# Performance work log

Hardware: AMD Instinct MI355X
Metric: run time of the kernel (lower is better)

## Reference

```python
import jax, jax.numpy as jnp
import numpy as np

E = 640000   # n_edges
D = 128      # feature_dim
N = 40000    # n_dst_nodes


def setup_inputs() -> dict:
    key = jax.random.key(0)
    k1, k2, k3 = jax.random.split(key, 3)
    src_emb = jax.random.normal(k1, (E, D), dtype=jnp.float32)
    dst_idx = jax.random.randint(k2, (E,), 0, N, dtype=jnp.int64)
    # nn.Linear default init scale ~ 1/sqrt(fan_in)
    W = jax.random.normal(k3, (D, D), dtype=jnp.float32) / jnp.sqrt(jnp.float32(D))
    b = jnp.zeros((D,), dtype=jnp.float32)
    return {"src_emb": src_emb, "W": W, "b": b, "dst_idx": dst_idx, "n_nodes": N}


def reference(src_emb, W, b, dst_idx, n_nodes):
    # msg_e = relu(Linear(src_emb))  -- per-edge messages [E, D]
    msg = jax.nn.relu(jnp.einsum("ed,fd->ef", src_emb, W) + b)
    # update_all(copy_edge, max) == segment max over destination nodes [N, D]
    h_node = jax.ops.segment_max(msg, dst_idx, num_segments=n_nodes)
    return h_node
```

## Files before the change

kernel.cpp:

```cpp
#include <hip/hip_runtime.h>
#include <hip/hip_bf16.h>

#define E_EDGES 640000
#define DIM     128
#define N_NODES 40000

typedef __bf16 bf16x8 __attribute__((ext_vector_type(8)));
typedef float  floatx4 __attribute__((ext_vector_type(4)));

__global__ void prep_kernel(const float* __restrict__ W,
                            __bf16* __restrict__ Wsw,
                            int* __restrict__ cnt) {
    int tid = blockIdx.x * blockDim.x + threadIdx.x;
    if (tid < N_NODES) cnt[tid] = 0;
    if (tid < 2048) {
        int lane = tid & 63;
        int kb   = (tid >> 6) & 3;
        int nb   = tid >> 8;
        int f    = nb * 16 + (lane & 15);
        int k0   = kb * 32 + ((lane >> 4) & 3) * 8;
        const float* wrow = W + f * DIM + k0;
        __bf16* o = Wsw + tid * 8;
#pragma unroll
        for (int j = 0; j < 8; ++j) o[j] = (__bf16)wrow[j];
    }
}

__global__ void hist_kernel(const int* __restrict__ dst, int* __restrict__ cnt) {
    int e = blockIdx.x * 256 + threadIdx.x;
    atomicAdd(&cnt[dst[e]], 1);
}

__global__ __launch_bounds__(1024)
void scan_kernel(const int* __restrict__ cnt, int* __restrict__ starts) {
    __shared__ int ssum[1024];
    const int t = threadIdx.x;
    const int base = t * 40;
    int local = 0;
#pragma unroll 4
    for (int i = 0; i < 40; ++i) {
        int idx = base + i;
        if (idx < N_NODES) local += cnt[idx];
    }
    ssum[t] = local;
    __syncthreads();
    for (int off = 1; off < 1024; off <<= 1) {
        int v = (t >= off) ? ssum[t - off] : 0;
        __syncthreads();
        ssum[t] += v;
        __syncthreads();
    }
    int run = ssum[t] - local;
    for (int i = 0; i < 40; ++i) {
        int idx = base + i;
        if (idx < N_NODES) { starts[idx] = run; run += cnt[idx]; }
    }
}

__global__ void scatter_kernel(const int* __restrict__ dst,
                               int* __restrict__ starts,
                               int* __restrict__ perm) {
    int e = blockIdx.x * 256 + threadIdx.x;
    int pos = atomicAdd(&starts[dst[e]], 1);
    perm[pos] = e;
}

__global__ __launch_bounds__(256)
void node_gemm_kernel(const float* __restrict__ src,
                      const __bf16* __restrict__ Wsw,
                      const float* __restrict__ bias,
                      const int* __restrict__ perm,
                      const int* __restrict__ cnt,
                      const int* __restrict__ ends,
                      float* __restrict__ out) {
    __shared__ bf16x8 Wl[2048];
    const int t = threadIdx.x;
    {
        const float4* gw = (const float4*)Wsw;
        float4* lw = (float4*)Wl;
#pragma unroll
        for (int i = 0; i < 8; ++i) lw[t + i * 256] = gw[t + i * 256];
    }
    __syncthreads();

    const int lane = t & 63;
    const int wave = t >> 6;
    const int q    = lane >> 4;
    const int n    = lane & 15;
    const int node = blockIdx.x * 4 + wave;

    const int c     = cnt[node];
    const int start = ends[node] - c;
    float* orow = out + (size_t)node * DIM;

    if (c == 0) {
        orow[lane]      = -INFINITY;
        orow[lane + 64] = -INFINITY;
        return;
    }

    floatx4 vmax[8];
#pragma unroll
    for (int nb = 0; nb < 8; ++nb) vmax[nb] = (floatx4)(-INFINITY);

    const int nch = (c + 15) >> 4;
    for (int ch = 0; ch < nch; ++ch) {
        int rows = c - (ch << 4);
        if (rows > 16) rows = 16;
        int e = (n < rows) ? perm[start + (ch << 4) + n] : 0;
        const float* arow = src + (size_t)e * DIM + q * 8;

        floatx4 acc[8];
#pragma unroll
        for (int nb = 0; nb < 8; ++nb) acc[nb] = (floatx4)(0.0f);

#pragma unroll
        for (int kb = 0; kb < 4; ++kb) {
            float4 a0 = *(const float4*)(arow + kb * 32);
            float4 a1 = *(const float4*)(arow + kb * 32 + 4);
            bf16x8 af;
            af[0] = (__bf16)a0.x; af[1] = (__bf16)a0.y;
            af[2] = (__bf16)a0.z; af[3] = (__bf16)a0.w;
            af[4] = (__bf16)a1.x; af[5] = (__bf16)a1.y;
            af[6] = (__bf16)a1.z; af[7] = (__bf16)a1.w;
#pragma unroll
            for (int nb = 0; nb < 8; ++nb) {
                bf16x8 bf = Wl[(nb * 4 + kb) * 64 + lane];
                acc[nb] = __builtin_amdgcn_mfma_f32_16x16x32_bf16(af, bf, acc[nb], 0, 0, 0);
            }
        }

#pragma unroll
        for (int nb = 0; nb < 8; ++nb) {
#pragma unroll
            for (int r = 0; r < 4; ++r) {
                float v = (q * 4 + r < rows) ? acc[nb][r] : -INFINITY;
                vmax[nb][r] = fmaxf(vmax[nb][r], v);
            }
        }
    }

    float red[8];
#pragma unroll
    for (int nb = 0; nb < 8; ++nb) {
        float v = fmaxf(fmaxf(vmax[nb][0], vmax[nb][1]),
                        fmaxf(vmax[nb][2], vmax[nb][3]));
        v = fmaxf(v, __shfl_xor(v, 16));
        v = fmaxf(v, __shfl_xor(v, 32));
        red[nb] = v;
    }

    float o1 = (q == 0) ? red[0] : (q == 1) ? red[1] : (q == 2) ? red[2] : red[3];
    float o2 = (q == 0) ? red[4] : (q == 1) ? red[5] : (q == 2) ? red[6] : red[7];

    orow[lane]      = fmaxf(o1 + bias[lane],      0.0f);
    orow[lane + 64] = fmaxf(o2 + bias[lane + 64], 0.0f);
}

extern "C" void kernel_launch(void* const* d_in, const int* in_sizes, int n_in,
                              void* d_out, int out_size, void* d_ws, size_t ws_size,
                              hipStream_t stream) {
    const float* src  = (const float*)d_in[0];
    const float* W    = (const float*)d_in[1];
    const float* bias = (const float*)d_in[2];
    const int*   dst  = (const int*)d_in[3];

    char* ws = (char*)d_ws;
    __bf16* Wsw  = (__bf16*)ws;
    int* cnt     = (int*)(ws + 32768);
    int* starts  = (int*)(ws + 32768 + 160000);
    int* perm    = (int*)(ws + 32768 + 320000);
    float* outf  = (float*)d_out;

    prep_kernel<<<(N_NODES + 255) / 256, 256, 0, stream>>>(W, Wsw, cnt);
    hist_kernel<<<E_EDGES / 256, 256, 0, stream>>>(dst, cnt);
    scan_kernel<<<1, 1024, 0, stream>>>(cnt, starts);
    scatter_kernel<<<E_EDGES / 256, 256, 0, stream>>>(dst, starts, perm);
    node_gemm_kernel<<<N_NODES / 4, 256, 0, stream>>>(src, Wsw, bias, perm,
                                                      cnt, starts, outf);
}
```

Measured before the change: 661.7 us.

## Fuse prep stages into cooperative kernel and persist GEMM waves with prefetch

Merges the zero/swizzle, histogram, scan and scatter kernels into one cooperative kernel with grid syncs, falling back to separate launches if the cooperative launch fails. The node GEMM becomes persistent: 1024 blocks loop over nodes with stride, prefetching the next node's count, start and first 32 edge indices while the current node's rows load, plus special-cased paths for nodes with up to 16 and up to 32 edges. The aim is to remove launch gaps and hide the latency of the dependent index gathers. The cost is grid-sync overhead, a single-block scan of 157 elements per thread, and fewer concurrent waves in the GEMM.

```diff
diff --git a/kernel.cpp b/kernel.cpp
--- a/kernel.cpp
+++ b/kernel.cpp
@@ -1,68 +1,162 @@
 #include <hip/hip_runtime.h>
 #include <hip/hip_bf16.h>
+#include <hip/hip_cooperative_groups.h>
+
+namespace cg = cooperative_groups;
 
 #define E_EDGES 640000
 #define DIM     128
 #define N_NODES 40000
 
+#define PREP_BLOCKS 1280
+#define PREP_THREADS (PREP_BLOCKS * 256)
+
+#define GEMM_BLOCKS 1024
+#define NWAVES_TOT  (GEMM_BLOCKS * 4)
+
 typedef __bf16 bf16x8 __attribute__((ext_vector_type(8)));
 typedef float  floatx4 __attribute__((ext_vector_type(4)));
+
+__device__ __forceinline__ void swizzle_w(const float* __restrict__ W,
+                                          __bf16* __restrict__ Wsw, int tid) {
+    int lane = tid & 63;
+    int kb   = (tid >> 6) & 3;
+    int nb   = tid >> 8;
+    int f    = nb * 16 + (lane & 15);
+    int k0   = kb * 32 + ((lane >> 4) & 3) * 8;
+    const float* wrow = W + f * DIM + k0;
+    __bf16* o = Wsw + tid * 8;
+#pragma unroll
+    for (int j = 0; j < 8; ++j) o[j] = (__bf16)wrow[j];
+}
+
+__global__ __launch_bounds__(256)
+void prep_all(const float* __restrict__ W, const int* __restrict__ dst,
+              __bf16* __restrict__ Wsw, int* __restrict__ cnt,
+              int* __restrict__ starts, int* __restrict__ perm) {
+    cg::grid_group grid = cg::this_grid();
+    __shared__ int ssum[256];
+    const int tid = blockIdx.x * 256 + threadIdx.x;
+
+    for (int i = tid; i < N_NODES; i += PREP_THREADS) cnt[i] = 0;
+    if (tid < 2048) swizzle_w(W, Wsw, tid);
+    grid.sync();
+
+    for (int e = tid; e < E_EDGES; e += PREP_THREADS) atomicAdd(&cnt[dst[e]], 1);
+    grid.sync();
+
+    if (blockIdx.x == 0) {
+        const int t = threadIdx.x;
+        const int base = t * 157;
+        int local = 0;
+        for (int i = 0; i < 157; ++i) {
+            int idx = base + i;
+            if (idx < N_NODES) local += cnt[idx];
+        }
+        ssum[t] = local;
+        __syncthreads();
+        for (int off = 1; off < 256; off <<= 1) {
+            int v = (t >= off) ? ssum[t - off] : 0;
+            __syncthreads();
+            ssum[t] += v;
+            __syncthreads();
+        }
+        int run = ssum[t] - local;
+        for (int i = 0; i < 157; ++i) {
+            int idx = base + i;
+            if (idx < N_NODES) { starts[idx] = run; run += cnt[idx]; }
+        }
+    }
+    grid.sync();
+
+    for (int e = tid; e < E_EDGES; e += PREP_THREADS) {
+        int pos = atomicAdd(&starts[dst[e]], 1);
+        perm[pos] = e;
+    }
+}
 
 __global__ void prep_kernel(const float* __restrict__ W,
                             __bf16* __restrict__ Wsw,
                             int* __restrict__ cnt) {
     int tid = blockIdx.x * blockDim.x + threadIdx.x;
     if (tid < N_NODES) cnt[tid] = 0;
-    if (tid < 2048) {
-        int lane = tid & 63;
-        int kb   = (tid >> 6) & 3;
-        int nb   = tid >> 8;
-        int f    = nb * 16 + (lane & 15);
-        int k0   = kb * 32 + ((lane >> 4) & 3) * 8;
-        const float* wrow = W + f * DIM + k0;
-        __bf16* o = Wsw + tid * 8;
-#pragma unroll
-        for (int j = 0; j < 8; ++j) o[j] = (__bf16)wrow[j];
-    }
-}
-
+    if (tid < 2048) swizzle_w(W, Wsw, tid);
+}
 __global__ void hist_kernel(const int* __restrict__ dst, int* __restrict__ cnt) {
     int e = blockIdx.x * 256 + threadIdx.x;
     atomicAdd(&cnt[dst[e]], 1);
 }
-
 __global__ __launch_bounds__(1024)
 void scan_kernel(const int* __restrict__ cnt, int* __restrict__ starts) {
-    __shared__ int ssum[1024];
+    __shared__ int ss[1024];
     const int t = threadIdx.x;
     const int base = t * 40;
     int local = 0;
-#pragma unroll 4
     for (int i = 0; i < 40; ++i) {
         int idx = base + i;
         if (idx < N_NODES) local += cnt[idx];
     }
-    ssum[t] = local;
+    ss[t] = local;
     __syncthreads();
     for (int off = 1; off < 1024; off <<= 1) {
-        int v = (t >= off) ? ssum[t - off] : 0;
+        int v = (t >= off) ? ss[t - off] : 0;
         __syncthreads();
-        ssum[t] += v;
+        ss[t] += v;
         __syncthreads();
     }
-    int run = ssum[t] - local;
+    int run = ss[t] - local;
     for (int i = 0; i < 40; ++i) {
         int idx = base + i;
         if (idx < N_NODES) { starts[idx] = run; run += cnt[idx]; }
     }
 }
-
 __global__ void scatter_kernel(const int* __restrict__ dst,
                                int* __restrict__ starts,
                                int* __restrict__ perm) {
     int e = blockIdx.x * 256 + threadIdx.x;
     int pos = atomicAdd(&starts[dst[e]], 1);
     perm[pos] = e;
+}
+
+__device__ __forceinline__ void load_convert(bf16x8 (&af)[4], const float* arow) {
+#pragma unroll
+    for (int kb = 0; kb < 4; ++kb) {
+        float4 a0 = *(const float4*)(arow + kb * 32);
+        float4 a1 = *(const float4*)(arow + kb * 32 + 4);
+        af[kb][0] = (__bf16)a0.x; af[kb][1] = (__bf16)a0.y;
+        af[kb][2] = (__bf16)a0.z; af[kb][3] = (__bf16)a0.w;
+        af[kb][4] = (__bf16)a1.x; af[kb][5] = (__bf16)a1.y;
+        af[kb][6] = (__bf16)a1.z; af[kb][7] = (__bf16)a1.w;
+    }
+}
+
+__device__ __forceinline__ void mfma_tile(const bf16x8 (&af)[4],
+                                          const bf16x8* __restrict__ Wl,
+                                          floatx4 (&acc)[8], int lane) {
+#pragma unroll
+    for (int kb = 0; kb < 4; ++kb)
+#pragma unroll
+        for (int nb = 0; nb < 8; ++nb)
+            acc[nb] = __builtin_amdgcn_mfma_f32_16x16x32_bf16(
+                af[kb], Wl[(nb * 4 + kb) * 64 + lane], acc[nb], 0, 0, 0);
+}
+
+__device__ __forceinline__ void reduce_store(floatx4 (&vm)[8],
+                                             const float* __restrict__ bias,
+                                             float* __restrict__ orow,
+                                             int q, int lane) {
+    float red[8];
+#pragma unroll
+    for (int nb = 0; nb < 8; ++nb) {
+        float v = fmaxf(fmaxf(vm[nb][0], vm[nb][1]), fmaxf(vm[nb][2], vm[nb][3]));
+        v = fmaxf(v, __shfl_xor(v, 16));
+        v = fmaxf(v, __shfl_xor(v, 32));
+        red[nb] = v;
+    }
+    float o1 = (q == 0) ? red[0] : (q == 1) ? red[1] : (q == 2) ? red[2] : red[3];
+    float o2 = (q == 0) ? red[4] : (q == 1) ? red[5] : (q == 2) ? red[6] : red[7];
+    orow[lane]      = fmaxf(o1 + bias[lane],      0.0f);
+    orow[lane + 64] = fmaxf(o2 + bias[lane + 64], 0.0f);
 }
 
 __global__ __launch_bounds__(256)
@@ -87,74 +181,103 @@
     const int wave = t >> 6;
     const int q    = lane >> 4;
     const int n    = lane & 15;
-    const int node = blockIdx.x * 4 + wave;
-
-    const int c     = cnt[node];
-    const int start = ends[node] - c;
-    float* orow = out + (size_t)node * DIM;
-
-    if (c == 0) {
-        orow[lane]      = -INFINITY;
-        orow[lane + 64] = -INFINITY;
-        return;
-    }
-
-    floatx4 vmax[8];
-#pragma unroll
-    for (int nb = 0; nb < 8; ++nb) vmax[nb] = (floatx4)(-INFINITY);
-
-    const int nch = (c + 15) >> 4;
-    for (int ch = 0; ch < nch; ++ch) {
-        int rows = c - (ch << 4);
-        if (rows > 16) rows = 16;
-        int e = (n < rows) ? perm[start + (ch << 4) + n] : 0;
-        const float* arow = src + (size_t)e * DIM + q * 8;
-
-        floatx4 acc[8];
-#pragma unroll
-        for (int nb = 0; nb < 8; ++nb) acc[nb] = (floatx4)(0.0f);
-
-#pragma unroll
-        for (int kb = 0; kb < 4; ++kb) {
-            float4 a0 = *(const float4*)(arow + kb * 32);
-            float4 a1 = *(const float4*)(arow + kb * 32 + 4);
-            bf16x8 af;
-            af[0] = (__bf16)a0.x; af[1] = (__bf16)a0.y;
-            af[2] = (__bf16)a0.z; af[3] = (__bf16)a0.w;
-            af[4] = (__bf16)a1.x; af[5] = (__bf16)a1.y;
-            af[6] = (__bf16)a1.z; af[7] = (__bf16)a1.w;
-#pragma unroll
-            for (int nb = 0; nb < 8; ++nb) {
-                bf16x8 bf = Wl[(nb * 4 + kb) * 64 + lane];
-                acc[nb] = __builtin_amdgcn_mfma_f32_16x16x32_bf16(af, bf, acc[nb], 0, 0, 0);
+
+    int node = blockIdx.x * 4 + wave;
+
+    int c  = cnt[node];
+    int st = ends[node] - c;
+    {
+        int r0 = c < 16 ? c : 16;
+        int r1 = (c > 16) ? ((c < 32 ? c : 32) - 16) : 0;
+        (void)r0; (void)r1;
+    }
+    int ea, eb;
+    {
+        int r0 = c < 16 ? c : 16;
+        ea = (n < r0) ? perm[st + n] : 0;
+        int r1 = (c > 16) ? ((c < 32 ? c : 32) - 16) : 0;
+        eb = (n < r1) ? perm[st + 16 + n] : 0;
+    }
+
+    while (true) {
+        const int nnode = node + NWAVES_TOT;
+        const bool hn = nnode < N_NODES;
+        int c2 = 0, st2 = 0, ea2 = 0, eb2 = 0;
+        if (hn) {
+            c2  = cnt[nnode];
+            st2 = ends[nnode] - c2;
+        }
+
+        bf16x8 af[4];
+        load_convert(af, src + (size_t)ea * DIM + q * 8);
+
+        if (hn) {
+            int r02 = c2 < 16 ? c2 : 16;
+            ea2 = (n < r02) ? perm[st2 + n] : 0;
+            int r12 = (c2 > 16) ? ((c2 < 32 ? c2 : 32) - 16) : 0;
+            eb2 = (n < r12) ? perm[st2 + 16 + n] : 0;
+        }
+
+        const int r1c = (c > 16) ? ((c < 32 ? c : 32) - 16) : 0;
+
+        float* orow = out + (size_t)node * DIM;
+        if (c == 0) {
+            orow[lane]      = -INFINITY;
+            orow[lane + 64] = -INFINITY;
+        } else {
+            floatx4 acc[8];
+#pragma unroll
+            for (int nb = 0; nb < 8; ++nb) acc[nb] = (floatx4)(0.0f);
+            mfma_tile(af, Wl, acc, lane);
+
+            if (c <= 16) {
+#pragma unroll
+                for (int nb = 0; nb < 8; ++nb)
+#pragma unroll
+                    for (int r = 0; r < 4; ++r)
+                        if (q * 4 + r >= c) acc[nb][r] = -INFINITY;
+                reduce_store(acc, bias, orow, q, lane);
+            } else {
+                floatx4 vmax[8];
+#pragma unroll
+                for (int nb = 0; nb < 8; ++nb) vmax[nb] = acc[nb];
+
+                bf16x8 af1[4];
+                load_convert(af1, src + (size_t)eb * DIM + q * 8);
+#pragma unroll
+                for (int nb = 0; nb < 8; ++nb) acc[nb] = (floatx4)(0.0f);
+                mfma_tile(af1, Wl, acc, lane);
+#pragma unroll
+                for (int nb = 0; nb < 8; ++nb)
+#pragma unroll
+                    for (int r = 0; r < 4; ++r) {
+                        float v = (q * 4 + r < r1c) ? acc[nb][r] : -INFINITY;
+                        vmax[nb][r] = fmaxf(vmax[nb][r], v);
+                    }
+
+                for (int base = 32; base < c; base += 16) {
+                    int rr = c - base; if (rr > 16) rr = 16;
+                    int e3 = (n < rr) ? perm[st + base + n] : 0;
+                    bf16x8 af2[4];
+                    load_convert(af2, src + (size_t)e3 * DIM + q * 8);
+#pragma unroll
+                    for (int nb = 0; nb < 8; ++nb) acc[nb] = (floatx4)(0.0f);
+                    mfma_tile(af2, Wl, acc, lane);
+#pragma unroll
+                    for (int nb = 0; nb < 8; ++nb)
+#pragma unroll
+                        for (int r = 0; r < 4; ++r) {
+                            float v = (q * 4 + r < rr) ? acc[nb][r] : -INFINITY;
+                            vmax[nb][r] = fmaxf(vmax[nb][r], v);
+                        }
+                }
+                reduce_store(vmax, bias, orow, q, lane);
             }
         }
 
-#pragma unroll
-        for (int nb = 0; nb < 8; ++nb) {
-#pragma unroll
-            for (int r = 0; r < 4; ++r) {
-                float v = (q * 4 + r < rows) ? acc[nb][r] : -INFINITY;
-                vmax[nb][r] = fmaxf(vmax[nb][r], v);
-            }
-        }
-    }
-
-    float red[8];
-#pragma unroll
-    for (int nb = 0; nb < 8; ++nb) {
-        float v = fmaxf(fmaxf(vmax[nb][0], vmax[nb][1]),
-                        fmaxf(vmax[nb][2], vmax[nb][3]));
-        v = fmaxf(v, __shfl_xor(v, 16));
-        v = fmaxf(v, __shfl_xor(v, 32));
-        red[nb] = v;
-    }
-
-    float o1 = (q == 0) ? red[0] : (q == 1) ? red[1] : (q == 2) ? red[2] : red[3];
-    float o2 = (q == 0) ? red[4] : (q == 1) ? red[5] : (q == 2) ? red[6] : red[7];
-
-    orow[lane]      = fmaxf(o1 + bias[lane],      0.0f);
-    orow[lane + 64] = fmaxf(o2 + bias[lane + 64], 0.0f);
+        if (!hn) break;
+        node = nnode; c = c2; st = st2; ea = ea2; eb = eb2;
+    }
 }
 
 extern "C" void kernel_launch(void* const* d_in, const int* in_sizes, int n_in,
@@ -172,10 +295,19 @@
     int* perm    = (int*)(ws + 32768 + 320000);
     float* outf  = (float*)d_out;
 
-    prep_kernel<<<(N_NODES + 255) / 256, 256, 0, stream>>>(W, Wsw, cnt);
-    hist_kernel<<<E_EDGES / 256, 256, 0, stream>>>(dst, cnt);
-    scan_kernel<<<1, 1024, 0, stream>>>(cnt, starts);
-    scatter_kernel<<<E_EDGES / 256, 256, 0, stream>>>(dst, starts, perm);
-    node_gemm_kernel<<<N_NODES / 4, 256, 0, stream>>>(src, Wsw, bias, perm,
+    void* kargs[] = {(void*)&W, (void*)&dst, (void*)&Wsw,
+                     (void*)&cnt, (void*)&starts, (void*)&perm};
+    hipError_t cerr = hipLaunchCooperativeKernel((const void*)prep_all,
+                                                 dim3(PREP_BLOCKS), dim3(256),
+                                                 kargs, 0, stream);
+    if (cerr != hipSuccess) {
+        (void)hipGetLastError();
+        prep_kernel<<<(N_NODES + 255) / 256, 256, 0, stream>>>(W, Wsw, cnt);
+        hist_kernel<<<E_EDGES / 256, 256, 0, stream>>>(dst, cnt);
+        scan_kernel<<<1, 1024, 0, stream>>>(cnt, starts);
+        scatter_kernel<<<E_EDGES / 256, 256, 0, stream>>>(dst, starts, perm);
+    }
+
+    node_gemm_kernel<<<GEMM_BLOCKS, 256, 0, stream>>>(src, Wsw, bias, perm,
                                                       cnt, starts, outf);
 }
```

After: 989.6 us. 49.6% more time.

## Replicate histogram 16-way and replace single-block scan with multi-block scan

Applied to the files above, without the earlier changes.

Builds the counting sort with 16 replicated histograms indexed by edge id modulo 16, which spreads atomic contention across copies. The single 1024-thread scan kernel is replaced by a three-stage multi-block scan (per-block sums, scan of block sums, per-node offsets), and that scan also writes per-replica start offsets for the scatter. The extra workspace and added launches cost something. The old path is kept as a fallback when the workspace is too small.

```diff
diff --git a/kernel.cpp b/kernel.cpp
--- a/kernel.cpp
+++ b/kernel.cpp
@@ -5,58 +5,146 @@
 #define DIM     128
 #define N_NODES 40000
 
+#define KREP  16
+#define HSIZE (KREP * N_NODES)
+
 typedef __bf16 bf16x8 __attribute__((ext_vector_type(8)));
 typedef float  floatx4 __attribute__((ext_vector_type(4)));
+
+__device__ __forceinline__ void swizzle_w(const float* __restrict__ W,
+                                          __bf16* __restrict__ Wsw, int tid) {
+    int lane = tid & 63;
+    int kb   = (tid >> 6) & 3;
+    int nb   = tid >> 8;
+    int f    = nb * 16 + (lane & 15);
+    int k0   = kb * 32 + ((lane >> 4) & 3) * 8;
+    const float* wrow = W + f * DIM + k0;
+    __bf16* o = Wsw + tid * 8;
+#pragma unroll
+    for (int j = 0; j < 8; ++j) o[j] = (__bf16)wrow[j];
+}
+
+__global__ void prep0_kernel(const float* __restrict__ W,
+                             __bf16* __restrict__ Wsw,
+                             int* __restrict__ H) {
+    int tid = blockIdx.x * 256 + threadIdx.x;
+    if (tid < HSIZE) H[tid] = 0;
+    if (tid < 2048) swizzle_w(W, Wsw, tid);
+}
+
+__global__ void hist16_kernel(const int* __restrict__ dst, int* __restrict__ H) {
+    int e = blockIdx.x * 256 + threadIdx.x;
+    atomicAdd(&H[(e & (KREP - 1)) * N_NODES + dst[e]], 1);
+}
+
+__global__ __launch_bounds__(256)
+void sum_kernel(const int* __restrict__ H, int* __restrict__ cnt,
+                int* __restrict__ bsum) {
+    __shared__ int sred[256];
+    int n = blockIdx.x * 256 + threadIdx.x;
+    int s = 0;
+    if (n < N_NODES) {
+#pragma unroll
+        for (int r = 0; r < KREP; ++r) s += H[r * N_NODES + n];
+        cnt[n] = s;
+    }
+    sred[threadIdx.x] = s;
+    __syncthreads();
+    for (int off = 128; off > 0; off >>= 1) {
+        if (threadIdx.x < off) sred[threadIdx.x] += sred[threadIdx.x + off];
+        __syncthreads();
+    }
+    if (threadIdx.x == 0) bsum[blockIdx.x] = sred[0];
+}
+
+__global__ __launch_bounds__(256)
+void scanb_kernel(const int* __restrict__ bsum, int* __restrict__ bstart) {
+    __shared__ int ss[256];
+    int t = threadIdx.x;
+    int v = (t < 160) ? bsum[t] : 0;
+    int orig = v;
+    ss[t] = v;
+    __syncthreads();
+    for (int off = 1; off < 256; off <<= 1) {
+        int u = (t >= off) ? ss[t - off] : 0;
+        __syncthreads();
+        ss[t] += u;
+        __syncthreads();
+    }
+    if (t < 160) bstart[t] = ss[t] - orig;
+}
+
+__global__ __launch_bounds__(256)
+void offs_kernel(int* __restrict__ H, const int* __restrict__ cnt,
+                 const int* __restrict__ bstart, int* __restrict__ starts) {
+    __shared__ int ss[256];
+    int t = threadIdx.x;
+    int n = blockIdx.x * 256 + t;
+    int v = (n < N_NODES) ? cnt[n] : 0;
+    int orig = v;
+    ss[t] = v;
+    __syncthreads();
+    for (int off = 1; off < 256; off <<= 1) {
+        int u = (t >= off) ? ss[t - off] : 0;
+        __syncthreads();
+        ss[t] += u;
+        __syncthreads();
+    }
+    if (n < N_NODES) {
+        int run = bstart[blockIdx.x] + ss[t] - orig;
+        starts[n] = run;
+#pragma unroll
+        for (int r = 0; r < KREP; ++r) {
+            int idx = r * N_NODES + n;
+            int h = H[idx];
+            H[idx] = run;
+            run += h;
+        }
+    }
+}
+
+__global__ void scatter16_kernel(const int* __restrict__ dst,
+                                 int* __restrict__ H, int* __restrict__ perm) {
+    int e = blockIdx.x * 256 + threadIdx.x;
+    int pos = atomicAdd(&H[(e & (KREP - 1)) * N_NODES + dst[e]], 1);
+    perm[pos] = e;
+}
 
 __global__ void prep_kernel(const float* __restrict__ W,
                             __bf16* __restrict__ Wsw,
                             int* __restrict__ cnt) {
     int tid = blockIdx.x * blockDim.x + threadIdx.x;
     if (tid < N_NODES) cnt[tid] = 0;
-    if (tid < 2048) {
-        int lane = tid & 63;
-        int kb   = (tid >> 6) & 3;
-        int nb   = tid >> 8;
-        int f    = nb * 16 + (lane & 15);
-        int k0   = kb * 32 + ((lane >> 4) & 3) * 8;
-        const float* wrow = W + f * DIM + k0;
-        __bf16* o = Wsw + tid * 8;
-#pragma unroll
-        for (int j = 0; j < 8; ++j) o[j] = (__bf16)wrow[j];
-    }
-}
-
+    if (tid < 2048) swizzle_w(W, Wsw, tid);
+}
 __global__ void hist_kernel(const int* __restrict__ dst, int* __restrict__ cnt) {
     int e = blockIdx.x * 256 + threadIdx.x;
     atomicAdd(&cnt[dst[e]], 1);
 }
-
 __global__ __launch_bounds__(1024)
 void scan_kernel(const int* __restrict__ cnt, int* __restrict__ starts) {
-    __shared__ int ssum[1024];
+    __shared__ int ss[1024];
     const int t = threadIdx.x;
     const int base = t * 40;
     int local = 0;
-#pragma unroll 4
     for (int i = 0; i < 40; ++i) {
         int idx = base + i;
         if (idx < N_NODES) local += cnt[idx];
     }
-    ssum[t] = local;
+    ss[t] = local;
     __syncthreads();
     for (int off = 1; off < 1024; off <<= 1) {
-        int v = (t >= off) ? ssum[t - off] : 0;
-        __syncthreads();
-        ssum[t] += v;
-        __syncthreads();
-    }
-    int run = ssum[t] - local;
+        int v = (t >= off) ? ss[t - off] : 0;
+        __syncthreads();
+        ss[t] += v;
+        __syncthreads();
+    }
+    int run = ss[t] - local;
     for (int i = 0; i < 40; ++i) {
         int idx = base + i;
         if (idx < N_NODES) { starts[idx] = run; run += cnt[idx]; }
     }
 }
-
 __global__ void scatter_kernel(const int* __restrict__ dst,
                                int* __restrict__ starts,
                                int* __restrict__ perm) {
@@ -71,8 +159,8 @@
                       const float* __restrict__ bias,
                       const int* __restrict__ perm,
                       const int* __restrict__ cnt,
-                      const int* __restrict__ ends,
-                      float* __restrict__ out) {
+                      const int* __restrict__ stends,
+                      float* __restrict__ out, int st_mode) {
     __shared__ bf16x8 Wl[2048];
     const int t = threadIdx.x;
     {
@@ -89,8 +177,9 @@
     const int n    = lane & 15;
     const int node = blockIdx.x * 4 + wave;
 
-    const int c     = cnt[node];
-    const int start = ends[node] - c;
+    const int c  = cnt[node];
+    const int se = stends[node];
+    const int st = st_mode ? (se - c) : se;
     float* orow = out + (size_t)node * DIM;
 
     if (c == 0) {
@@ -107,7 +196,7 @@
     for (int ch = 0; ch < nch; ++ch) {
         int rows = c - (ch << 4);
         if (rows > 16) rows = 16;
-        int e = (n < rows) ? perm[start + (ch << 4) + n] : 0;
+        int e = (n < rows) ? perm[st + (ch << 4) + n] : 0;
         const float* arow = src + (size_t)e * DIM + q * 8;
 
         floatx4 acc[8];
@@ -131,13 +220,12 @@
         }
 
 #pragma unroll
-        for (int nb = 0; nb < 8; ++nb) {
+        for (int nb = 0; nb < 8; ++nb)
 #pragma unroll
             for (int r = 0; r < 4; ++r) {
                 float v = (q * 4 + r < rows) ? acc[nb][r] : -INFINITY;
                 vmax[nb][r] = fmaxf(vmax[nb][r], v);
             }
-        }
     }
 
     float red[8];
@@ -149,10 +237,8 @@
         v = fmaxf(v, __shfl_xor(v, 32));
         red[nb] = v;
     }
-
     float o1 = (q == 0) ? red[0] : (q == 1) ? red[1] : (q == 2) ? red[2] : red[3];
     float o2 = (q == 0) ? red[4] : (q == 1) ? red[5] : (q == 2) ? red[6] : red[7];
-
     orow[lane]      = fmaxf(o1 + bias[lane],      0.0f);
     orow[lane + 64] = fmaxf(o2 + bias[lane + 64], 0.0f);
 }
@@ -166,16 +252,31 @@
     const int*   dst  = (const int*)d_in[3];
 
     char* ws = (char*)d_ws;
-    __bf16* Wsw  = (__bf16*)ws;
-    int* cnt     = (int*)(ws + 32768);
-    int* starts  = (int*)(ws + 32768 + 160000);
-    int* perm    = (int*)(ws + 32768 + 320000);
+    size_t off = 0;
+    __bf16* Wsw  = (__bf16*)(ws + off); off += 32768;
+    int* cnt     = (int*)(ws + off);    off += 160000;
+    int* starts  = (int*)(ws + off);    off += 160000;
+    int* perm    = (int*)(ws + off);    off += 2560000;
+    int* bsum    = (int*)(ws + off);    off += 1024;
+    int* bstart  = (int*)(ws + off);    off += 1024;
+    int* H       = (int*)(ws + off);    off += (size_t)HSIZE * 4;
     float* outf  = (float*)d_out;
 
-    prep_kernel<<<(N_NODES + 255) / 256, 256, 0, stream>>>(W, Wsw, cnt);
-    hist_kernel<<<E_EDGES / 256, 256, 0, stream>>>(dst, cnt);
-    scan_kernel<<<1, 1024, 0, stream>>>(cnt, starts);
-    scatter_kernel<<<E_EDGES / 256, 256, 0, stream>>>(dst, starts, perm);
-    node_gemm_kernel<<<N_NODES / 4, 256, 0, stream>>>(src, Wsw, bias, perm,
-                                                      cnt, starts, outf);
-}
+    if (ws_size >= off) {
+        prep0_kernel<<<2500, 256, 0, stream>>>(W, Wsw, H);
+        hist16_kernel<<<E_EDGES / 256, 256, 0, stream>>>(dst, H);
+        sum_kernel<<<160, 256, 0, stream>>>(H, cnt, bsum);
+        scanb_kernel<<<1, 256, 0, stream>>>(bsum, bstart);
+        offs_kernel<<<160, 256, 0, stream>>>(H, cnt, bstart, starts);
+        scatter16_kernel<<<E_EDGES / 256, 256, 0, stream>>>(dst, H, perm);
+        node_gemm_kernel<<<N_NODES / 4, 256, 0, stream>>>(src, Wsw, bias, perm,
+                                                          cnt, starts, outf, 0);
+    } else {
+        prep_kernel<<<(N_NODES + 255) / 256, 256, 0, stream>>>(W, Wsw, cnt);
+        hist_kernel<<<E_EDGES / 256, 256, 0, stream>>>(dst, cnt);
+        scan_kernel<<<1, 1024, 0, stream>>>(cnt, starts);
+        scatter_kernel<<<E_EDGES / 256, 256, 0, stream>>>(dst, starts, perm);
+        node_gemm_kernel<<<N_NODES / 4, 256, 0, stream>>>(src, Wsw, bias, perm,
+                                                          cnt, starts, outf, 1);
+    }
+}
```

Result: faster. 603.0 us (-8.9%).
